# Performance work log

Measured on AMD Instinct MI355X. Metric: run time of the kernel, lower is better.

Reference implementation:

```python
import jax, jax.numpy as jnp
import numpy as np

N = 10000        # nodes
E = 640000       # edges (before self-loops)
D_IN = 128
D_OUT = 128
NEG_SLOPE = 0.2  # PyG GATConv default


def setup_inputs() -> dict:
    key = jax.random.key(0)
    k1, k2, k3, k4, k5 = jax.random.split(key, 5)
    x = jax.random.normal(k1, (N, D_IN), dtype=jnp.float32)
    edge_index = jax.random.randint(k2, (2, E), 0, N, dtype=jnp.int64)
    # learned params of GATConv(in, out, heads=1)
    W = jax.random.normal(k3, (D_IN, D_OUT), dtype=jnp.float32) / np.sqrt(D_IN).astype(np.float32)
    att_src = jax.random.normal(k4, (D_OUT,), dtype=jnp.float32) * 0.1
    att_dst = jax.random.normal(k5, (D_OUT,), dtype=jnp.float32) * 0.1
    bias = jnp.zeros((D_OUT,), dtype=jnp.float32)
    return {"x": x, "W": W, "att_src": att_src, "att_dst": att_dst,
            "bias": bias, "edge_index": edge_index}


def reference(x, W, att_src, att_dst, bias, edge_index):
    # PyG GATConv default: add self-loops
    loop = jnp.arange(N, dtype=edge_index.dtype)
    src = jnp.concatenate([edge_index[0], loop])  # [E+N]
    dst = jnp.concatenate([edge_index[1], loop])  # [E+N]

    h = x @ W                          # [N, D_OUT]
    a_s = h @ att_src                  # [N] per-node source logit
    a_d = h @ att_dst                  # [N] per-node dest logit

    # per-edge attention logits, LeakyReLU(0.2)
    e = jax.nn.leaky_relu(a_s[src] + a_d[dst], negative_slope=NEG_SLOPE)  # [E+N]

    # segment softmax over incoming edges of each destination node
    m = jax.ops.segment_max(e, dst, num_segments=N)       # [N]
    m = jax.lax.stop_gradient(m)
    ex = jnp.exp(e - m[dst])
    denom = jax.ops.segment_sum(ex, dst, num_segments=N)  # [N]
    alpha = ex / denom[dst]                                # [E+N]

    # weighted scatter-aggregate of transformed source features
    msgs = alpha[:, None] * h[src]                         # [E+N, D_OUT]
    out = jax.ops.segment_sum(msgs, dst, num_segments=N)   # [N, D_OUT]
    return out + bias
```

## Files before the change

### kernel.cpp

```cpp
#include <hip/hip_runtime.h>
#include <hip/hip_bf16.h>

#define N_NODES 10000
#define E_EDGES 640000
#define D_IN 128
#define D_OUT 128
#define NEG_SLOPE 0.2f

#define BSH 3
#define NBIN 1250
#define NFB 256
#define FCHUNK 2500
#define RSTRIDE 1280
#define DCAP 160

typedef unsigned short ushort_t;
typedef unsigned int uint_t;
typedef __attribute__((ext_vector_type(8))) short short8;
typedef __attribute__((ext_vector_type(4))) float v4f;

static __device__ __forceinline__ float bf2f(uint_t u) {
  return __uint_as_float(u << 16);
}
static __device__ __forceinline__ ushort_t f2bf(float f) {
  unsigned int x = __float_as_uint(f);
  return (ushort_t)((x + 0x7fffu + ((x >> 16) & 1u)) >> 16);
}

union SmemU {
  struct {
    ushort_t Wt[128 * 132];
    float asum[16], dsum[16];
  } g;
  struct {
    int hist[NBIN];
    int cur[NBIN];
    int scanA[256], scanB[256];
    int sortedL[FCHUNK];
  } f;
};

__global__ __launch_bounds__(256) void gat_main(
    const float* __restrict__ x, const float* __restrict__ W,
    const float* __restrict__ att_src, const float* __restrict__ att_dst,
    const int* __restrict__ src, const int* __restrict__ dst,
    ushort_t* __restrict__ hb, float* __restrict__ a_s, float* __restrict__ a_d,
    int* __restrict__ sortedg, int2* __restrict__ runinfo) {
  __shared__ SmemU sm;
  const int t = threadIdx.x;

  if (blockIdx.x < NFB) {
    const int b = blockIdx.x;
    const int4* s4 = reinterpret_cast<const int4*>(src + b * FCHUNK);
    const int4* d4 = reinterpret_cast<const int4*>(dst + b * FCHUNK);
    for (int i = t; i < NBIN; i += 256) sm.f.hist[i] = 0;

    int4 sv[3], dv[3];
    #pragma unroll
    for (int it = 0; it < 3; ++it) {
      const int i = t + it * 256;
      if (i < FCHUNK / 4) { sv[it] = s4[i]; dv[it] = d4[i]; }
    }
    __syncthreads();

    #pragma unroll
    for (int it = 0; it < 3; ++it) {
      const int i = t + it * 256;
      if (i < FCHUNK / 4) {
        atomicAdd(&sm.f.hist[dv[it].x >> BSH], 1);
        atomicAdd(&sm.f.hist[dv[it].y >> BSH], 1);
        atomicAdd(&sm.f.hist[dv[it].z >> BSH], 1);
        atomicAdd(&sm.f.hist[dv[it].w >> BSH], 1);
      }
    }
    __syncthreads();

    int localv[5];
    int ssum = 0;
    #pragma unroll
    for (int j = 0; j < 5; ++j) {
      const int bb = 5 * t + j;
      const int v = (bb < NBIN) ? sm.f.hist[bb] : 0;
      localv[j] = ssum;
      ssum += v;
    }
    sm.f.scanA[t] = ssum;
    __syncthreads();
    int* pa = sm.f.scanA;
    int* pb = sm.f.scanB;
    for (int off = 1; off < 256; off <<= 1) {
      int s = pa[t];
      if (t >= off) s += pa[t - off];
      pb[t] = s;
      __syncthreads();
      int* tmp = pa; pa = pb; pb = tmp;
    }
    const int excl = pa[t] - ssum;
    #pragma unroll
    for (int j = 0; j < 5; ++j) {
      const int bb = 5 * t + j;
      if (bb < NBIN) sm.f.cur[bb] = excl + localv[j];
    }
    __syncthreads();

    #pragma unroll
    for (int it = 0; it < 3; ++it) {
      const int i = t + it * 256;
      if (i < FCHUNK / 4) {
        #pragma unroll
        for (int j = 0; j < 4; ++j) {
          const int s = (j == 0) ? sv[it].x : (j == 1) ? sv[it].y
                      : (j == 2) ? sv[it].z : sv[it].w;
          const int d = (j == 0) ? dv[it].x : (j == 1) ? dv[it].y
                      : (j == 2) ? dv[it].z : dv[it].w;
          const int rel = atomicAdd(&sm.f.cur[d >> BSH], 1);
          sm.f.sortedL[rel] = s | ((d & 7) << 14);
        }
      }
    }
    __syncthreads();

    const int4* sl4 = reinterpret_cast<const int4*>(sm.f.sortedL);
    int4* sg4 = reinterpret_cast<int4*>(sortedg + (size_t)b * FCHUNK);
    for (int i = t; i < FCHUNK / 4; i += 256) sg4[i] = sl4[i];
    for (int k = t; k < NBIN; k += 256)
      runinfo[b * RSTRIDE + k] =
          make_int2(b * FCHUNK + sm.f.cur[k] - sm.f.hist[k], sm.f.hist[k]);

  } else {
    const int l = t & 63, w = t >> 6;
    const int ln16 = l & 15, kg = l >> 4;
    const int r0 = (blockIdx.x - NFB) * 16;
    const int k0base = kg * 8;

    {
      const int c = t & 127;
      const int khb = (t >> 7) * 4;
      for (int kb = khb; kb < 128; kb += 8) {
        const float f0 = W[(kb + 0) * D_OUT + c];
        const float f1 = W[(kb + 1) * D_OUT + c];
        const float f2 = W[(kb + 2) * D_OUT + c];
        const float f3 = W[(kb + 3) * D_OUT + c];
        const uint_t p0 = (uint_t)f2bf(f0) | ((uint_t)f2bf(f1) << 16);
        const uint_t p1 = (uint_t)f2bf(f2) | ((uint_t)f2bf(f3) << 16);
        *reinterpret_cast<uint_t*>(&sm.g.Wt[c * 132 + kb]) = p0;
        *reinterpret_cast<uint_t*>(&sm.g.Wt[c * 132 + kb + 2]) = p1;
      }
    }
    if (t < 16) { sm.g.asum[t] = 0.f; sm.g.dsum[t] = 0.f; }

    short8 afrag[4];
    #pragma unroll
    for (int kt = 0; kt < 4; ++kt) {
      const int k0 = kt * 32 + k0base;
      const float4* xp = reinterpret_cast<const float4*>(
          x + (size_t)(r0 + ln16) * D_IN + k0);
      const float4 x0 = xp[0], x1 = xp[1];
      short8 af;
      af[0] = (short)f2bf(x0.x); af[1] = (short)f2bf(x0.y);
      af[2] = (short)f2bf(x0.z); af[3] = (short)f2bf(x0.w);
      af[4] = (short)f2bf(x1.x); af[5] = (short)f2bf(x1.y);
      af[6] = (short)f2bf(x1.z); af[7] = (short)f2bf(x1.w);
      afrag[kt] = af;
    }
    __syncthreads();

    const int cb0 = w * 32, cb1 = w * 32 + 16;
    v4f acc0 = {0.f, 0.f, 0.f, 0.f};
    v4f acc1 = {0.f, 0.f, 0.f, 0.f};
    #pragma unroll
    for (int kt = 0; kt < 4; ++kt) {
      const int k0 = kt * 32 + k0base;
      union { uint2 q[2]; short8 s; } b0, b1;
      b0.q[0] = *reinterpret_cast<const uint2*>(&sm.g.Wt[(cb0 + ln16) * 132 + k0]);
      b0.q[1] = *reinterpret_cast<const uint2*>(&sm.g.Wt[(cb0 + ln16) * 132 + k0 + 4]);
      b1.q[0] = *reinterpret_cast<const uint2*>(&sm.g.Wt[(cb1 + ln16) * 132 + k0]);
      b1.q[1] = *reinterpret_cast<const uint2*>(&sm.g.Wt[(cb1 + ln16) * 132 + k0 + 4]);
      acc0 = __builtin_amdgcn_mfma_f32_16x16x32_bf16(afrag[kt], b0.s, acc0, 0, 0, 0);
      acc1 = __builtin_amdgcn_mfma_f32_16x16x32_bf16(afrag[kt], b1.s, acc1, 0, 0, 0);
    }

    const float ats0 = att_src[cb0 + ln16], ats1 = att_src[cb1 + ln16];
    const float atd0 = att_dst[cb0 + ln16], atd1 = att_dst[cb1 + ln16];
    #pragma unroll
    for (int reg = 0; reg < 4; ++reg) {
      const int R = kg * 4 + reg;
      hb[(size_t)(r0 + R) * D_OUT + cb0 + ln16] = f2bf(acc0[reg]);
      hb[(size_t)(r0 + R) * D_OUT + cb1 + ln16] = f2bf(acc1[reg]);
      float ps = acc0[reg] * ats0 + acc1[reg] * ats1;
      float pd = acc0[reg] * atd0 + acc1[reg] * atd1;
      #pragma unroll
      for (int off = 8; off >= 1; off >>= 1) {
        ps += __shfl_xor(ps, off, 16);
        pd += __shfl_xor(pd, off, 16);
      }
      if (ln16 == 0) {
        atomicAdd(&sm.g.asum[R], ps);
        atomicAdd(&sm.g.dsum[R], pd);
      }
    }
    __syncthreads();
    if (t < 16) { a_s[r0 + t] = sm.g.asum[t]; a_d[r0 + t] = sm.g.dsum[t]; }
  }
}

__global__ __launch_bounds__(256, 4) void gat_aggregate(
    const ushort_t* __restrict__ hb, const int* __restrict__ sortedg,
    const int2* __restrict__ runinfo, const float* __restrict__ a_s,
    const float* __restrict__ a_d, const float* __restrict__ bias,
    float* __restrict__ out) {
  __shared__ int2 seg[8 * DCAP];
  __shared__ float adl[8];
  __shared__ int curs[8];
  const int j = blockIdx.x, t = threadIdx.x;
  const int hw = t >> 5, ln = t & 31;

  if (t < 8) { curs[t] = 0; adl[t] = a_d[j * 8 + t]; }
  const int2 ri = runinfo[t * RSTRIDE + j];
  __syncthreads();

  {
    int r = 0;
    while (r < ri.y) {
      const int nb = min(ri.y - r, 8);
      int rec[8];
      float av[8];
      #pragma unroll
      for (int u = 0; u < 8; ++u)
        if (u < nb) rec[u] = sortedg[ri.x + r + u];
      #pragma unroll
      for (int u = 0; u < 8; ++u)
        if (u < nb) av[u] = a_s[rec[u] & 16383];
      #pragma unroll
      for (int u = 0; u < 8; ++u)
        if (u < nb) {
          const int dl = (rec[u] >> 14) & 7;
          float lv = av[u] + adl[dl];
          lv = fmaxf(lv, NEG_SLOPE * lv);
          const int pos = atomicAdd(&curs[dl], 1);
          if (pos < DCAP)
            seg[dl * DCAP + pos] =
                make_int2(rec[u] & 16383, __float_as_int(__expf(lv)));
        }
      r += nb;
    }
  }
  __syncthreads();

  const int d = j * 8 + hw;
  const int cnt = min(curs[hw], DCAP);
  const int2* sj = &seg[hw * DCAP];
  const char* hbase = (const char*)hb + ln * 8;
  float ax = 0.f, ay = 0.f, az = 0.f, aw = 0.f, sex = 0.f;
  int i = 0;
  for (; i + 8 <= cnt; i += 8) {
    int2 p[8];
    *reinterpret_cast<int4*>(&p[0]) = *reinterpret_cast<const int4*>(&sj[i]);
    *reinterpret_cast<int4*>(&p[2]) = *reinterpret_cast<const int4*>(&sj[i + 2]);
    *reinterpret_cast<int4*>(&p[4]) = *reinterpret_cast<const int4*>(&sj[i + 4]);
    *reinterpret_cast<int4*>(&p[6]) = *reinterpret_cast<const int4*>(&sj[i + 6]);
    ushort4 hv[8];
    #pragma unroll
    for (int u = 0; u < 8; ++u)
      hv[u] = *reinterpret_cast<const ushort4*>(
          hbase + (size_t)(p[u].x) * 256);
    #pragma unroll
    for (int u = 0; u < 8; ++u) {
      const float e = __int_as_float(p[u].y);
      ax += e * bf2f(hv[u].x); ay += e * bf2f(hv[u].y);
      az += e * bf2f(hv[u].z); aw += e * bf2f(hv[u].w);
      sex += e;
    }
  }
  for (; i < cnt; ++i) {
    const int2 p = sj[i];
    const float e = __int_as_float(p.y);
    const ushort4 hu = *reinterpret_cast<const ushort4*>(
        hbase + (size_t)(p.x) * 256);
    ax += e * bf2f(hu.x); ay += e * bf2f(hu.y);
    az += e * bf2f(hu.z); aw += e * bf2f(hu.w);
    sex += e;
  }
  float lv = a_s[d] + adl[hw];
  lv = lv > 0.f ? lv : NEG_SLOPE * lv;
  const float es = __expf(lv);
  const ushort4 hs = *reinterpret_cast<const ushort4*>(hbase + (size_t)d * 256);
  ax += es * bf2f(hs.x); ay += es * bf2f(hs.y);
  az += es * bf2f(hs.z); aw += es * bf2f(hs.w);
  sex += es;

  const float4 bv = reinterpret_cast<const float4*>(bias)[ln];
  const float inv = 1.f / sex;
  reinterpret_cast<float4*>(out)[(size_t)d * 32 + ln] =
      make_float4(ax * inv + bv.x, ay * inv + bv.y,
                  az * inv + bv.z, aw * inv + bv.w);
}

extern "C" void kernel_launch(void* const* d_in, const int* in_sizes, int n_in,
                              void* d_out, int out_size, void* d_ws, size_t ws_size,
                              hipStream_t stream) {
  const float* x       = (const float*)d_in[0];
  const float* W       = (const float*)d_in[1];
  const float* att_src = (const float*)d_in[2];
  const float* att_dst = (const float*)d_in[3];
  const float* bias    = (const float*)d_in[4];
  const int*   ei      = (const int*)d_in[5];
  const int* src = ei;
  const int* dst = ei + E_EDGES;
  float* out = (float*)d_out;

  char* ws = (char*)d_ws;
  ushort_t* hb      = (ushort_t*)(ws);
  float*    a_s     = (float*)(ws + 2560000);
  float*    a_d     = (float*)(ws + 2600000);
  int*      sortedg = (int*)  (ws + 2640000);
  int2*     runinfo = (int2*) (ws + 5200000);

  gat_main<<<NFB + 625, 256, 0, stream>>>(x, W, att_src, att_dst, src, dst,
                                          hb, a_s, a_d, sortedg, runinfo);

  gat_aggregate<<<NBIN, 256, 0, stream>>>(hb, sortedg, runinfo,
                                          a_s, a_d, bias, out);
}
```

Measured before the change: 39.81 us.

## Pack run info into 32-bit words, remap blocks per XCD, nontemporal output stores

Run descriptors are packed from int2 into a single 32-bit word holding the offset and count, which halves the bytes written and read for the run table. The aggregate kernel's block index is remapped so that consecutive destination bins land on the same XCD, which should improve L2 locality for the shared hb rows and sortedg data. Output stores become nontemporal so they do not pollute the cache. The packing relies on each offset and count fitting in 16 bits, which holds for FCHUNK=2500.

New measurement: 36.93 us. -7.2%, faster.

```diff
diff --git a/kernel.cpp b/kernel.cpp
--- a/kernel.cpp
+++ b/kernel.cpp
@@ -45,7 +45,7 @@
     const float* __restrict__ att_src, const float* __restrict__ att_dst,
     const int* __restrict__ src, const int* __restrict__ dst,
     ushort_t* __restrict__ hb, float* __restrict__ a_s, float* __restrict__ a_d,
-    int* __restrict__ sortedg, int2* __restrict__ runinfo) {
+    int* __restrict__ sortedg, uint_t* __restrict__ runinfo) {
   __shared__ SmemU sm;
   const int t = threadIdx.x;
 
@@ -125,7 +125,7 @@
     for (int i = t; i < FCHUNK / 4; i += 256) sg4[i] = sl4[i];
     for (int k = t; k < NBIN; k += 256)
       runinfo[b * RSTRIDE + k] =
-          make_int2(b * FCHUNK + sm.f.cur[k] - sm.f.hist[k], sm.f.hist[k]);
+          (uint_t)(sm.f.cur[k] - sm.f.hist[k]) | ((uint_t)sm.f.hist[k] << 16);
 
   } else {
     const int l = t & 63, w = t >> 6;
@@ -206,28 +206,32 @@
 
 __global__ __launch_bounds__(256, 4) void gat_aggregate(
     const ushort_t* __restrict__ hb, const int* __restrict__ sortedg,
-    const int2* __restrict__ runinfo, const float* __restrict__ a_s,
+    const uint_t* __restrict__ runinfo, const float* __restrict__ a_s,
     const float* __restrict__ a_d, const float* __restrict__ bias,
     float* __restrict__ out) {
   __shared__ int2 seg[8 * DCAP];
   __shared__ float adl[8];
   __shared__ int curs[8];
-  const int j = blockIdx.x, t = threadIdx.x;
+  const int B = blockIdx.x, t = threadIdx.x;
+  const int xcd = B & 7, idx = B >> 3;
+  const int j = (xcd < 2 ? xcd * 157 : 314 + (xcd - 2) * 156) + idx;
   const int hw = t >> 5, ln = t & 31;
 
   if (t < 8) { curs[t] = 0; adl[t] = a_d[j * 8 + t]; }
-  const int2 ri = runinfo[t * RSTRIDE + j];
+  const uint_t riU = runinfo[t * RSTRIDE + j];
   __syncthreads();
 
   {
+    const int rbase = t * FCHUNK + (int)(riU & 0xffffu);
+    const int rcnt = (int)(riU >> 16);
     int r = 0;
-    while (r < ri.y) {
-      const int nb = min(ri.y - r, 8);
+    while (r < rcnt) {
+      const int nb = min(rcnt - r, 8);
       int rec[8];
       float av[8];
       #pragma unroll
       for (int u = 0; u < 8; ++u)
-        if (u < nb) rec[u] = sortedg[ri.x + r + u];
+        if (u < nb) rec[u] = sortedg[rbase + r + u];
       #pragma unroll
       for (int u = 0; u < 8; ++u)
         if (u < nb) av[u] = a_s[rec[u] & 16383];
@@ -291,9 +295,11 @@
 
   const float4 bv = reinterpret_cast<const float4*>(bias)[ln];
   const float inv = 1.f / sex;
-  reinterpret_cast<float4*>(out)[(size_t)d * 32 + ln] =
-      make_float4(ax * inv + bv.x, ay * inv + bv.y,
-                  az * inv + bv.z, aw * inv + bv.w);
+  v4f ov;
+  ov[0] = ax * inv + bv.x; ov[1] = ay * inv + bv.y;
+  ov[2] = az * inv + bv.z; ov[3] = aw * inv + bv.w;
+  __builtin_nontemporal_store(ov, reinterpret_cast<v4f*>(out) +
+                                      (size_t)d * 32 + ln);
 }
 
 extern "C" void kernel_launch(void* const* d_in, const int* in_sizes, int n_in,
@@ -314,7 +320,7 @@
   float*    a_s     = (float*)(ws + 2560000);
   float*    a_d     = (float*)(ws + 2600000);
   int*      sortedg = (int*)  (ws + 2640000);
-  int2*     runinfo = (int2*) (ws + 5200000);
+  uint_t*   runinfo = (uint_t*)(ws + 5200000);
 
   gat_main<<<NFB + 625, 256, 0, stream>>>(x, W, att_src, att_dst, src, dst,
                                           hb, a_s, a_d, sortedg, runinfo);
```
